# Optimization experiments

Hardware: AMD Instinct MI355X
Metric: run time of the kernel (lower is better)

Reference implementation:

```python
import jax, jax.numpy as jnp
import numpy as np

N_HEAD = 16
N_KV = 4
HEAD_DIM = 64
QK_SCALE = 1.2
VE_GATE_CH = 12


def rms_norm(x):
    # F.rms_norm with default eps = finfo(dtype).eps, no learned scale
    eps = jnp.asarray(jnp.finfo(x.dtype).eps, x.dtype)
    return x * jax.lax.rsqrt(jnp.mean(x * x, axis=-1, keepdims=True) + eps)


def apply_rotary(x, cos, sin):
    # x: (B,T,H,D); cos/sin: (1,T,1,D//2)
    d = x.shape[-1] // 2
    x1, x2 = x[..., :d], x[..., d:]
    return jnp.concatenate([x1 * cos + x2 * sin, -x1 * sin + x2 * cos], axis=-1)


def setup_inputs() -> dict:
    key = jax.random.key(0)
    ks = jax.random.split(key, 8)
    B, T, C = 2, 2048, 1024
    x = jax.random.normal(ks[0], (B, T, C), jnp.float32)
    ve = jax.random.normal(ks[1], (B, T, N_KV * HEAD_DIM), jnp.float32)
    # realistic rotary tables for positions 0..T
    half = HEAD_DIM // 2
    inv_freq = 1.0 / (10000.0 ** (np.arange(half, dtype=np.float64) / half))
    ang = np.arange(T)[:, None] * inv_freq[None, :]
    cos = jnp.asarray(np.cos(ang), jnp.float32)[None, :, None, :]
    sin = jnp.asarray(np.sin(ang), jnp.float32)[None, :, None, :]
    s = 0.02
    Wq = jax.random.normal(ks[2], (N_HEAD * HEAD_DIM, C), jnp.float32) * s
    Wk = jax.random.normal(ks[3], (N_KV * HEAD_DIM, C), jnp.float32) * s
    Wv = jax.random.normal(ks[4], (N_KV * HEAD_DIM, C), jnp.float32) * s
    Wo = jax.random.normal(ks[5], (C, C), jnp.float32) * s
    Wg = jax.random.normal(ks[6], (N_KV, VE_GATE_CH), jnp.float32) * s
    return dict(x=x, ve=ve, cos=cos, sin=sin, Wq=Wq, Wk=Wk, Wv=Wv, Wo=Wo,
                Wg=Wg, window_left=1024)


def reference(x, ve, cos, sin, Wq, Wk, Wv, Wo, Wg, window_left):
    B, T, C = x.shape
    G = N_HEAD // N_KV  # GQA group size
    q = (x @ Wq.T).reshape(B, T, N_HEAD, HEAD_DIM)
    k = (x @ Wk.T).reshape(B, T, N_KV, HEAD_DIM)
    v = (x @ Wv.T).reshape(B, T, N_KV, HEAD_DIM)
    # sigmoid-gated value-embedding mixing
    gate = 3.0 * jax.nn.sigmoid(x[..., :VE_GATE_CH] @ Wg.T)  # (B,T,N_KV)
    v = v + gate[..., None] * ve.reshape(B, T, N_KV, HEAD_DIM)
    # RoPE -> RMSNorm -> qk_scale on both q and k
    q = rms_norm(apply_rotary(q, cos, sin)) * QK_SCALE
    k = rms_norm(apply_rotary(k, cos, sin)) * QK_SCALE
    # GQA attention with causal + sliding window (flash default scale 1/sqrt(d))
    qg = q.reshape(B, T, N_KV, G, HEAD_DIM)
    scale = 1.0 / jnp.sqrt(jnp.asarray(HEAD_DIM, q.dtype))
    scores = jnp.einsum('bqkgd,bskd->bkgqs', qg, k) * scale  # (B,N_KV,G,T,T)
    i = jnp.arange(T)[:, None]
    j = jnp.arange(T)[None, :]
    mask = (j <= i) & (i - j <= window_left)
    scores = jnp.where(mask, scores, jnp.asarray(-1e30, scores.dtype))
    attn = jax.nn.softmax(scores, axis=-1)
    y = jnp.einsum('bkgqs,bskd->bqkgd', attn, v).reshape(B, T, N_HEAD * HEAD_DIM)
    return y @ Wo.T
```

## Files before the change

kernel.cpp:

```cpp
#include <hip/hip_runtime.h>
#include <hip/hip_bf16.h>

#define B_ 2
#define T_ 2048
#define C_ 1024
#define NH 16
#define NKV 4
#define HD 64
#define NQKV 1536
#define KVB 64

typedef __attribute__((ext_vector_type(4))) float f32x4;
typedef __attribute__((ext_vector_type(8))) short bf16x8;
typedef __attribute__((ext_vector_type(4))) short bf16x4;

__device__ __forceinline__ unsigned short f2bf(float f) {
  __hip_bfloat16 h = __float2bfloat16(f);
  unsigned short u;
  __builtin_memcpy(&u, &h, 2);
  return u;
}

__device__ __forceinline__ void gload16(const void* g, void* l) {
  __builtin_amdgcn_global_load_lds(
      (const __attribute__((address_space(1))) void*)g,
      (__attribute__((address_space(3))) void*)l, 16, 0, 0);
}

__device__ __forceinline__ unsigned cvtpk(float lo, float hi_) {
  unsigned w;
  asm("v_cvt_pk_bf16_f32 %0, %1, %2" : "=v"(w) : "v"(lo), "v"(hi_));
  return w;
}

#define NX4  1048576
#define NW4  262144
#define NK4  65536
#define O1 (NX4)
#define O2 (O1 + NW4)
#define O3 (O2 + NK4)
#define O4 (O3 + NK4)
#define OT (O4 + NW4)

__global__ __launch_bounds__(256) void conv_all(
    const float* __restrict__ x, const float* __restrict__ wq, const float* __restrict__ wk,
    const float* __restrict__ wv, const float* __restrict__ wo,
    unsigned short* __restrict__ xb, unsigned short* __restrict__ wqkvb,
    unsigned short* __restrict__ wob) {
  int i = blockIdx.x * blockDim.x + threadIdx.x;
  const int stride = gridDim.x * blockDim.x;
  for (; i < OT; i += stride) {
    const float* src;
    unsigned short* dst;
    int j;
    if (i < O1)      { src = x;  dst = xb;                    j = i; }
    else if (i < O2) { src = wq; dst = wqkvb;                 j = i - O1; }
    else if (i < O3) { src = wk; dst = wqkvb + 1024 * 1024;   j = i - O2; }
    else if (i < O4) { src = wv; dst = wqkvb + 1280 * 1024;   j = i - O3; }
    else             { src = wo; dst = wob;                   j = i - O4; }
    const float4 v = reinterpret_cast<const float4*>(src)[j];
    ushort4 o;
    o.x = f2bf(v.x); o.y = f2bf(v.y); o.z = f2bf(v.z); o.w = f2bf(v.w);
    reinterpret_cast<ushort4*>(dst)[j] = o;
  }
}

#define BK 64

__global__ __launch_bounds__(256) void gemm_qkv(
    const unsigned short* __restrict__ A, const unsigned short* __restrict__ Bw,
    const float* __restrict__ x, const float* __restrict__ ve,
    const float* __restrict__ cosb, const float* __restrict__ sinb,
    const float* __restrict__ Wg,
    unsigned short* __restrict__ Qn, unsigned short* __restrict__ Kn,
    unsigned short* __restrict__ Vt) {
  constexpr int BMT = 128, MI = 4, NI = 2, K = 1024;
  __shared__ char smem[50176];
  unsigned short* AlB = (unsigned short*)smem;
  unsigned short* BlB = (unsigned short*)(smem + 32768);
  const int tid = threadIdx.x;
  const int lane = tid & 63;
  const int wid = tid >> 6;
  const int r = lane & 15, g = lane >> 4;
  const int wm = (wid >> 1) * 64, wn = (wid & 1) * 32;
  const int bm0 = blockIdx.y * BMT, bn0 = blockIdx.x * 64;
  const int lrow = lane >> 3;
  const int lcol = ((lane & 7) ^ lrow) * 8;
  const unsigned short* Asrc = A + (size_t)(bm0 + wid * 32 + lrow) * K + lcol;
  const unsigned short* Bsrc = Bw + (size_t)(bn0 + wid * 16 + lrow) * K + lcol;
  const int fsw = (r & 7) << 4;
  f32x4 acc[MI][NI] = {};

  auto stage = [&](int k0, int buf) {
#pragma unroll
    for (int i = 0; i < 4; ++i)
      gload16(Asrc + (size_t)(i * 8) * K + k0, AlB + buf * 8192 + (wid * 32 + i * 8) * BK);
#pragma unroll
    for (int i = 0; i < 2; ++i)
      gload16(Bsrc + (size_t)(i * 8) * K + k0, BlB + buf * 4096 + (wid * 16 + i * 8) * BK);
  };

  stage(0, 0);
  __syncthreads();
  const int nt = K / BK;
  for (int t = 0; t < nt; ++t) {
    const int cur = t & 1;
    if (t + 1 < nt) stage((t + 1) * BK, cur ^ 1);
    const char* Ac = (const char*)(AlB + cur * 8192);
    const char* Bc = (const char*)(BlB + cur * 4096);
    bf16x8 af[MI][2], bfr[NI][2];
#pragma unroll
    for (int mi = 0; mi < MI; ++mi)
#pragma unroll
      for (int s = 0; s < 2; ++s)
        af[mi][s] = *reinterpret_cast<const bf16x8*>(
            Ac + (wm + mi * 16 + r) * 128 + ((s * 64 + g * 16) ^ fsw));
#pragma unroll
    for (int ni = 0; ni < NI; ++ni)
#pragma unroll
      for (int s = 0; s < 2; ++s)
        bfr[ni][s] = *reinterpret_cast<const bf16x8*>(
            Bc + (wn + ni * 16 + r) * 128 + ((s * 64 + g * 16) ^ fsw));
#pragma unroll
    for (int s = 0; s < 2; ++s)
#pragma unroll
      for (int mi = 0; mi < MI; ++mi)
#pragma unroll
        for (int ni = 0; ni < NI; ++ni)
          acc[mi][ni] = __builtin_amdgcn_mfma_f32_16x16x32_bf16(af[mi][s], bfr[ni][s],
                                                                acc[mi][ni], 0, 0, 0);
    __syncthreads();
  }
  float* Cl = (float*)smem;
  unsigned short* Vst = (unsigned short*)(smem + 33280);
#pragma unroll
  for (int mi = 0; mi < MI; ++mi)
#pragma unroll
    for (int ni = 0; ni < NI; ++ni)
#pragma unroll
      for (int e = 0; e < 4; ++e)
        Cl[(wm + mi * 16 + g * 4 + e) * 65 + wn + ni * 16 + r] = acc[mi][ni][e];
  __syncthreads();
  const int head = blockIdx.x;
  const int trow = tid >> 1, half = tid & 1;
  const int tg = bm0 + trow;
  const int b = tg >> 11, t = tg & 2047;
  if (head < 20) {
    float r1[16], r2[16];
    float sq = 0.f;
#pragma unroll
    for (int i = 0; i < 16; ++i) {
      const int d = half * 16 + i;
      const float x1 = Cl[trow * 65 + d];
      const float x2 = Cl[trow * 65 + d + 32];
      const float c = cosb[t * 32 + d];
      const float s = sinb[t * 32 + d];
      r1[i] = x1 * c + x2 * s;
      r2[i] = x2 * c - x1 * s;
      sq += r1[i] * r1[i] + r2[i] * r2[i];
    }
    sq += __shfl_xor(sq, 1);
    const float sc = rsqrtf(sq * (1.0f / 64.0f) + 1.1920929e-7f) *
                     ((head < 16) ? 0.21640425613334453f : 1.2f);
    unsigned short* dst = (head < 16)
        ? Qn + (((size_t)b * NH + head) * T_ + t) * HD
        : Kn + (((size_t)b * NKV + (head - 16)) * T_ + t) * HD;
#pragma unroll
    for (int i4 = 0; i4 < 4; ++i4) {
      ushort4 w1, w2;
      w1.x = f2bf(r1[i4 * 4 + 0] * sc); w1.y = f2bf(r1[i4 * 4 + 1] * sc);
      w1.z = f2bf(r1[i4 * 4 + 2] * sc); w1.w = f2bf(r1[i4 * 4 + 3] * sc);
      w2.x = f2bf(r2[i4 * 4 + 0] * sc); w2.y = f2bf(r2[i4 * 4 + 1] * sc);
      w2.z = f2bf(r2[i4 * 4 + 2] * sc); w2.w = f2bf(r2[i4 * 4 + 3] * sc);
      *reinterpret_cast<ushort4*>(dst + half * 16 + i4 * 4) = w1;
      *reinterpret_cast<ushort4*>(dst + half * 16 + 32 + i4 * 4) = w2;
    }
  } else {
    const int kv = head - 20;
    float dot = 0.f;
#pragma unroll
    for (int i = 0; i < 12; ++i) dot += x[(size_t)tg * C_ + i] * Wg[kv * 12 + i];
    const float gate = 3.0f / (1.0f + __expf(-dot));
    const float* vsrc = ve + (size_t)tg * (NKV * HD) + kv * HD;
#pragma unroll
    for (int i = 0; i < 32; ++i) {
      const int d = half * 32 + i;
      Vst[d * 128 + trow] = f2bf(Cl[trow * 65 + d] + gate * vsrc[d]);
    }
    __syncthreads();
    const int dd = tid >> 2, t0 = (tid & 3) * 32;
    unsigned short* vd = Vt + (((size_t)b * NKV + kv) * HD + dd) * T_ + (bm0 & 2047) + t0;
    const unsigned short* vs2 = Vst + dd * 128 + t0;
#pragma unroll
    for (int i = 0; i < 4; ++i)
      *reinterpret_cast<bf16x8*>(vd + i * 8) = *reinterpret_cast<const bf16x8*>(vs2 + i * 8);
  }
}

template <int BMT, int BNT, bool OUTBF>
__global__ __launch_bounds__(256) void gemm_bt(const unsigned short* __restrict__ A,
                                               const unsigned short* __restrict__ Bw,
                                               void* __restrict__ Cv, int M, int N, int K) {
  constexpr int MI = BMT / 32;
  constexpr int NI = BNT / 32;
  __shared__ unsigned short Al[2][BMT * BK];
  __shared__ unsigned short Bl[2][BNT * BK];
  const int tid = threadIdx.x;
  const int lane = tid & 63;
  const int wid = tid >> 6;
  const int r = lane & 15, g = lane >> 4;
  const int wm = (wid >> 1) * (BMT / 2), wn = (wid & 1) * (BNT / 2);
  const int bm0 = blockIdx.y * BMT, bn0 = blockIdx.x * BNT;
  const int lrow = lane >> 3;
  const int lcol = ((lane & 7) ^ lrow) * 8;
  const unsigned short* Asrc = A + (size_t)(bm0 + wid * (BMT / 4) + lrow) * K + lcol;
  const unsigned short* Bsrc = Bw + (size_t)(bn0 + wid * (BNT / 4) + lrow) * K + lcol;
  const int fsw = (r & 7) << 4;
  f32x4 acc[MI][NI] = {};

  auto stage = [&](int k0, int buf) {
#pragma unroll
    for (int i = 0; i < BMT / 32; ++i)
      gload16(Asrc + (size_t)(i * 8) * K + k0, Al[buf] + (wid * (BMT / 4) + i * 8) * BK);
#pragma unroll
    for (int i = 0; i < BNT / 32; ++i)
      gload16(Bsrc + (size_t)(i * 8) * K + k0, Bl[buf] + (wid * (BNT / 4) + i * 8) * BK);
  };

  stage(0, 0);
  __syncthreads();
  const int nt = K / BK;
  for (int t = 0; t < nt; ++t) {
    const int cur = t & 1;
    if (t + 1 < nt) stage((t + 1) * BK, cur ^ 1);
    const char* Ac = (const char*)Al[cur];
    const char* Bc = (const char*)Bl[cur];
    bf16x8 af[MI][2], bfr[NI][2];
#pragma unroll
    for (int mi = 0; mi < MI; ++mi)
#pragma unroll
      for (int s = 0; s < 2; ++s)
        af[mi][s] = *reinterpret_cast<const bf16x8*>(
            Ac + (wm + mi * 16 + r) * 128 + ((s * 64 + g * 16) ^ fsw));
#pragma unroll
    for (int ni = 0; ni < NI; ++ni)
#pragma unroll
      for (int s = 0; s < 2; ++s)
        bfr[ni][s] = *reinterpret_cast<const bf16x8*>(
            Bc + (wn + ni * 16 + r) * 128 + ((s * 64 + g * 16) ^ fsw));
#pragma unroll
    for (int s = 0; s < 2; ++s)
#pragma unroll
      for (int mi = 0; mi < MI; ++mi)
#pragma unroll
        for (int ni = 0; ni < NI; ++ni)
          acc[mi][ni] = __builtin_amdgcn_mfma_f32_16x16x32_bf16(af[mi][s], bfr[ni][s],
                                                                acc[mi][ni], 0, 0, 0);
    __syncthreads();
  }
#pragma unroll
  for (int mi = 0; mi < MI; ++mi)
#pragma unroll
    for (int ni = 0; ni < NI; ++ni) {
      const int row = bm0 + wm + mi * 16 + g * 4;
      const int col = bn0 + wn + ni * 16 + r;
#pragma unroll
      for (int e = 0; e < 4; ++e) {
        if (OUTBF)
          ((unsigned short*)Cv)[(size_t)(row + e) * N + col] = f2bf(acc[mi][ni][e]);
        else
          ((float*)Cv)[(size_t)(row + e) * N + col] = acc[mi][ni][e];
      }
    }
}

__global__ __launch_bounds__(256, 4) void attn_fwd(
    const unsigned short* __restrict__ Qn, const unsigned short* __restrict__ Kn,
    const unsigned short* __restrict__ Vt, unsigned short* __restrict__ Y,
    const int* __restrict__ wlp) {
  __shared__ unsigned short Kl[2][KVB * 64];
  __shared__ unsigned short Vl[2][64 * KVB];
  __shared__ unsigned short Pl[4][16 * 64];
  const int j = blockIdx.x, h = blockIdx.y, b = blockIdx.z;
  const int kvh = h >> 2;
  const int tid = threadIdx.x;
  const int wid = tid >> 6, lane = tid & 63;
  const int r = lane & 15, g = lane >> 4;
  const int wl = *wlp;
  const unsigned short* Kb = Kn + (size_t)(b * NKV + kvh) * T_ * HD;
  const unsigned short* Vb = Vt + (size_t)(b * NKV + kvh) * HD * T_;
  const int srow = tid >> 3;
  const int scolb = (tid & 7) * 16;
  const int sdst = srow * 128 + (scolb ^ ((srow & 7) << 4));
  const unsigned short* Ksrc0 = Kb + (size_t)srow * HD + (scolb >> 1);
  const unsigned short* Ksrc1 = Kb + (size_t)(srow + 32) * HD + (scolb >> 1);
  const unsigned short* Vsrc0 = Vb + (size_t)srow * T_ + (scolb >> 1);
  const unsigned short* Vsrc1 = Vb + (size_t)(srow + 32) * T_ + (scolb >> 1);
  char* Pwb = (char*)Pl[wid];
  const int swz = (r & 7) << 4;
  const int ksw = swz;
  const int nseg = (j < 8) ? 2 : 1;

  for (int seg = 0; seg < nseg; ++seg) {
    const int qt = (j < 8) ? (seg ? 15 - j : j) : j + 8;
    const int q0 = qt * 64;
    const int qs = q0 + wid * 16;
    const int q = qs + r;
    const unsigned short* Qb = Qn + ((size_t)(b * NH + h) * T_ + qs) * HD;
    const bf16x8 qf0 = *reinterpret_cast<const bf16x8*>(Qb + r * HD + g * 8);
    const bf16x8 qf1 = *reinterpret_cast<const bf16x8*>(Qb + r * HD + 32 + g * 8);
    float lrun = 0.f;
    f32x4 o[4] = {};
    int slo = q0 - wl; if (slo < 0) slo = 0;
    slo &= ~63;
    const int send = q0 + 63;

    bf16x8 ska, skb, sva, svb;
    ska = *reinterpret_cast<const bf16x8*>(Ksrc0 + (size_t)slo * HD);
    skb = *reinterpret_cast<const bf16x8*>(Ksrc1 + (size_t)slo * HD);
    sva = *reinterpret_cast<const bf16x8*>(Vsrc0 + slo);
    svb = *reinterpret_cast<const bf16x8*>(Vsrc1 + slo);
    {
      char* Kd = (char*)Kl[0]; char* Vd = (char*)Vl[0];
      *reinterpret_cast<bf16x8*>(Kd + sdst) = ska;
      *reinterpret_cast<bf16x8*>(Kd + 32 * 128 + sdst) = skb;
      *reinterpret_cast<bf16x8*>(Vd + sdst) = sva;
      *reinterpret_cast<bf16x8*>(Vd + 32 * 128 + sdst) = svb;
    }
    __syncthreads();

    int cur = 0;
    for (int sb = slo; sb <= send; sb += KVB) {
      const bool has_next = (sb + KVB <= send);
      if (has_next) {
        const int nb = sb + KVB;
        ska = *reinterpret_cast<const bf16x8*>(Ksrc0 + (size_t)nb * HD);
        skb = *reinterpret_cast<const bf16x8*>(Ksrc1 + (size_t)nb * HD);
        sva = *reinterpret_cast<const bf16x8*>(Vsrc0 + nb);
        svb = *reinterpret_cast<const bf16x8*>(Vsrc1 + nb);
      }
      {
        const char* Kc = (const char*)Kl[cur];
        const char* Vc = (const char*)Vl[cur];
        float sv[16];
        __builtin_amdgcn_s_setprio(1);
#pragma unroll
        for (int sub = 0; sub < 4; ++sub) {
          const int rowb = (sub * 16 + r) * 128;
          bf16x8 kf0 = *reinterpret_cast<const bf16x8*>(Kc + rowb + ((g * 16) ^ ksw));
          bf16x8 kf1 = *reinterpret_cast<const bf16x8*>(Kc + rowb + ((64 + g * 16) ^ ksw));
          f32x4 z = {};
          z = __builtin_amdgcn_mfma_f32_16x16x32_bf16(kf0, qf0, z, 0, 0, 0);
          z = __builtin_amdgcn_mfma_f32_16x16x32_bf16(kf1, qf1, z, 0, 0, 0);
#pragma unroll
          for (int e = 0; e < 4; ++e) sv[sub * 4 + e] = z[e];
        }
        __builtin_amdgcn_s_setprio(0);
        if (sb + 63 > qs || sb < qs + 15 - wl) {
#pragma unroll
          for (int i = 0; i < 16; ++i) {
            const int s_ = sb + (i >> 2) * 16 + g * 4 + (i & 3);
            const bool ok = (unsigned)(q - s_) <= (unsigned)wl;
            sv[i] = ok ? sv[i] : -__builtin_inff();
          }
        }
        float pe[16];
        float ps = 0.f;
#pragma unroll
        for (int i = 0; i < 16; ++i) {
          pe[i] = __builtin_amdgcn_exp2f(sv[i] - 17.0f);
          ps += pe[i];
        }
        lrun += ps;
#pragma unroll
        for (int sub = 0; sub < 4; ++sub) {
          unsigned w2[2];
          w2[0] = cvtpk(pe[sub * 4 + 0], pe[sub * 4 + 1]);
          w2[1] = cvtpk(pe[sub * 4 + 2], pe[sub * 4 + 3]);
          bf16x4 w;
          __builtin_memcpy(&w, w2, 8);
          *reinterpret_cast<bf16x4*>(Pwb + ((r * 128 + sub * 32 + g * 8) ^ swz)) = w;
        }
        asm volatile("s_waitcnt lgkmcnt(0)" ::: "memory");
        __builtin_amdgcn_s_setprio(1);
#pragma unroll
        for (int c = 0; c < 2; ++c) {
          const bf16x8 pf = *reinterpret_cast<const bf16x8*>(Pwb + ((r * 128 + c * 64 + g * 16) ^ swz));
#pragma unroll
          for (int dt = 0; dt < 4; ++dt) {
            const int vrow = (dt * 16 + r) * 128;
            const bf16x8 vf = *reinterpret_cast<const bf16x8*>(Vc + vrow + ((c * 64 + g * 16) ^ ksw));
            o[dt] = __builtin_amdgcn_mfma_f32_16x16x32_bf16(vf, pf, o[dt], 0, 0, 0);
          }
        }
        __builtin_amdgcn_s_setprio(0);
      }
      if (has_next) {
        char* Kd = (char*)Kl[cur ^ 1]; char* Vd = (char*)Vl[cur ^ 1];
        *reinterpret_cast<bf16x8*>(Kd + sdst) = ska;
        *reinterpret_cast<bf16x8*>(Kd + 32 * 128 + sdst) = skb;
        *reinterpret_cast<bf16x8*>(Vd + sdst) = sva;
        *reinterpret_cast<bf16x8*>(Vd + 32 * 128 + sdst) = svb;
      }
      __syncthreads();
      cur ^= 1;
    }
    lrun += __shfl_xor(lrun, 16);
    lrun += __shfl_xor(lrun, 32);
    const float inv = 1.0f / lrun;
    unsigned short* Yb = Y + ((size_t)(b * T_) + qs + r) * (NH * HD) + h * HD;
#pragma unroll
    for (int dt = 0; dt < 4; ++dt)
#pragma unroll
      for (int e = 0; e < 4; ++e)
        Yb[dt * 16 + g * 4 + e] = f2bf(o[dt][e] * inv);
  }
}

extern "C" void kernel_launch(void* const* d_in, const int* in_sizes, int n_in,
                              void* d_out, int out_size, void* d_ws, size_t ws_size,
                              hipStream_t stream) {
  const float* x    = (const float*)d_in[0];
  const float* ve   = (const float*)d_in[1];
  const float* cosb = (const float*)d_in[2];
  const float* sinb = (const float*)d_in[3];
  const float* Wq   = (const float*)d_in[4];
  const float* Wk   = (const float*)d_in[5];
  const float* Wv   = (const float*)d_in[6];
  const float* Wo   = (const float*)d_in[7];
  const float* Wg   = (const float*)d_in[8];
  const int*   wlp  = (const int*)d_in[9];

  char* ws = (char*)d_ws;
  unsigned short* xb    = (unsigned short*)ws; ws += (size_t)4096 * 1024 * 2;
  unsigned short* wqkvb = (unsigned short*)ws; ws += (size_t)1536 * 1024 * 2;
  unsigned short* wob   = (unsigned short*)ws; ws += (size_t)1024 * 1024 * 2;
  unsigned short* Qn    = (unsigned short*)ws; ws += (size_t)B_ * NH * T_ * HD * 2;
  unsigned short* Kn    = (unsigned short*)ws; ws += (size_t)B_ * NKV * T_ * HD * 2;
  unsigned short* Vt    = (unsigned short*)ws; ws += (size_t)B_ * NKV * HD * T_ * 2;
  unsigned short* yb    = (unsigned short*)ws; ws += (size_t)4096 * 1024 * 2;

  conv_all<<<dim3(2048), dim3(256), 0, stream>>>(x, Wq, Wk, Wv, Wo, xb, wqkvb, wob);

  gemm_qkv<<<dim3(NQKV / 64, 4096 / 128), dim3(256), 0, stream>>>(
      xb, wqkvb, x, ve, cosb, sinb, Wg, Qn, Kn, Vt);

  attn_fwd<<<dim3(24, NH, B_), dim3(256), 0, stream>>>(Qn, Kn, Vt, yb, wlp);

  gemm_bt<128, 64, false><<<dim3(1024 / 64, 4096 / 128), dim3(256), 0, stream>>>(
      yb, wob, d_out, 4096, 1024, 1024);
}
```

Measured before the change: 76.26 us.

## Fuse x fp32-to-bf16 conversion into QKV GEMM A-tile loading

New measurement: 84.34 us. 1.11x slower.

```diff
diff --git a/kernel.cpp b/kernel.cpp
--- a/kernel.cpp
+++ b/kernel.cpp
@@ -33,31 +33,27 @@
   return w;
 }
 
-#define NX4  1048576
 #define NW4  262144
 #define NK4  65536
-#define O1 (NX4)
-#define O2 (O1 + NW4)
-#define O3 (O2 + NK4)
-#define O4 (O3 + NK4)
-#define OT (O4 + NW4)
+#define W1 (NW4)
+#define W2 (W1 + NK4)
+#define W3 (W2 + NK4)
+#define WT (W3 + NW4)
 
 __global__ __launch_bounds__(256) void conv_all(
-    const float* __restrict__ x, const float* __restrict__ wq, const float* __restrict__ wk,
+    const float* __restrict__ wq, const float* __restrict__ wk,
     const float* __restrict__ wv, const float* __restrict__ wo,
-    unsigned short* __restrict__ xb, unsigned short* __restrict__ wqkvb,
-    unsigned short* __restrict__ wob) {
+    unsigned short* __restrict__ wqkvb, unsigned short* __restrict__ wob) {
   int i = blockIdx.x * blockDim.x + threadIdx.x;
   const int stride = gridDim.x * blockDim.x;
-  for (; i < OT; i += stride) {
+  for (; i < WT; i += stride) {
     const float* src;
     unsigned short* dst;
     int j;
-    if (i < O1)      { src = x;  dst = xb;                    j = i; }
-    else if (i < O2) { src = wq; dst = wqkvb;                 j = i - O1; }
-    else if (i < O3) { src = wk; dst = wqkvb + 1024 * 1024;   j = i - O2; }
-    else if (i < O4) { src = wv; dst = wqkvb + 1280 * 1024;   j = i - O3; }
-    else             { src = wo; dst = wob;                   j = i - O4; }
+    if (i < W1)      { src = wq; dst = wqkvb;                 j = i; }
+    else if (i < W2) { src = wk; dst = wqkvb + 1024 * 1024;   j = i - W1; }
+    else if (i < W3) { src = wv; dst = wqkvb + 1280 * 1024;   j = i - W2; }
+    else             { src = wo; dst = wob;                   j = i - W3; }
     const float4 v = reinterpret_cast<const float4*>(src)[j];
     ushort4 o;
     o.x = f2bf(v.x); o.y = f2bf(v.y); o.z = f2bf(v.z); o.w = f2bf(v.w);
@@ -68,8 +64,8 @@
 #define BK 64
 
 __global__ __launch_bounds__(256) void gemm_qkv(
-    const unsigned short* __restrict__ A, const unsigned short* __restrict__ Bw,
-    const float* __restrict__ x, const float* __restrict__ ve,
+    const float* __restrict__ x, const unsigned short* __restrict__ Bw,
+    const float* __restrict__ ve,
     const float* __restrict__ cosb, const float* __restrict__ sinb,
     const float* __restrict__ Wg,
     unsigned short* __restrict__ Qn, unsigned short* __restrict__ Kn,
@@ -85,27 +81,49 @@
   const int wm = (wid >> 1) * 64, wn = (wid & 1) * 32;
   const int bm0 = blockIdx.y * BMT, bn0 = blockIdx.x * 64;
   const int lrow = lane >> 3;
-  const int lcol = ((lane & 7) ^ lrow) * 8;
-  const unsigned short* Asrc = A + (size_t)(bm0 + wid * 32 + lrow) * K + lcol;
+  const int lslot = lane & 7;
+  const int lcol = (lslot ^ lrow) * 8;
   const unsigned short* Bsrc = Bw + (size_t)(bn0 + wid * 16 + lrow) * K + lcol;
   const int fsw = (r & 7) << 4;
   f32x4 acc[MI][NI] = {};
 
-  auto stage = [&](int k0, int buf) {
-#pragma unroll
-    for (int i = 0; i < 4; ++i)
-      gload16(Asrc + (size_t)(i * 8) * K + k0, AlB + buf * 8192 + (wid * 32 + i * 8) * BK);
+  float4 a0[4], a1[4];
+  const float* Axs = x + (size_t)(bm0 + wid * 32 + lrow) * K + lslot * 8;
+  const int adst0 = (wid * 32 + lrow) * 128 + ((lslot * 16) ^ (lrow << 4));
+
+  auto loadA = [&](int k0) {
+#pragma unroll
+    for (int i = 0; i < 4; ++i) {
+      const float* src = Axs + (size_t)(i * 8) * K + k0;
+      a0[i] = *reinterpret_cast<const float4*>(src);
+      a1[i] = *reinterpret_cast<const float4*>(src + 4);
+    }
+  };
+  auto writeA = [&](int buf) {
+    char* base = (char*)(AlB + buf * 8192);
+#pragma unroll
+    for (int i = 0; i < 4; ++i) {
+      unsigned w[4];
+      w[0] = cvtpk(a0[i].x, a0[i].y); w[1] = cvtpk(a0[i].z, a0[i].w);
+      w[2] = cvtpk(a1[i].x, a1[i].y); w[3] = cvtpk(a1[i].z, a1[i].w);
+      bf16x8 v; __builtin_memcpy(&v, w, 16);
+      *reinterpret_cast<bf16x8*>(base + adst0 + i * 8 * 128) = v;
+    }
+  };
+  auto stageB = [&](int k0, int buf) {
 #pragma unroll
     for (int i = 0; i < 2; ++i)
       gload16(Bsrc + (size_t)(i * 8) * K + k0, BlB + buf * 4096 + (wid * 16 + i * 8) * BK);
   };
 
-  stage(0, 0);
+  loadA(0);
+  stageB(0, 0);
+  writeA(0);
   __syncthreads();
   const int nt = K / BK;
   for (int t = 0; t < nt; ++t) {
     const int cur = t & 1;
-    if (t + 1 < nt) stage((t + 1) * BK, cur ^ 1);
+    if (t + 1 < nt) { loadA((t + 1) * BK); stageB((t + 1) * BK, cur ^ 1); }
     const char* Ac = (const char*)(AlB + cur * 8192);
     const char* Bc = (const char*)(BlB + cur * 4096);
     bf16x8 af[MI][2], bfr[NI][2];
@@ -129,6 +147,7 @@
         for (int ni = 0; ni < NI; ++ni)
           acc[mi][ni] = __builtin_amdgcn_mfma_f32_16x16x32_bf16(af[mi][s], bfr[ni][s],
                                                                 acc[mi][ni], 0, 0, 0);
+    if (t + 1 < nt) writeA(cur ^ 1);
     __syncthreads();
   }
   float* Cl = (float*)smem;
@@ -432,7 +451,6 @@
   const int*   wlp  = (const int*)d_in[9];
 
   char* ws = (char*)d_ws;
-  unsigned short* xb    = (unsigned short*)ws; ws += (size_t)4096 * 1024 * 2;
   unsigned short* wqkvb = (unsigned short*)ws; ws += (size_t)1536 * 1024 * 2;
   unsigned short* wob   = (unsigned short*)ws; ws += (size_t)1024 * 1024 * 2;
   unsigned short* Qn    = (unsigned short*)ws; ws += (size_t)B_ * NH * T_ * HD * 2;
@@ -440,10 +458,10 @@
   unsigned short* Vt    = (unsigned short*)ws; ws += (size_t)B_ * NKV * HD * T_ * 2;
   unsigned short* yb    = (unsigned short*)ws; ws += (size_t)4096 * 1024 * 2;
 
-  conv_all<<<dim3(2048), dim3(256), 0, stream>>>(x, Wq, Wk, Wv, Wo, xb, wqkvb, wob);
+  conv_all<<<dim3(1024), dim3(256), 0, stream>>>(Wq, Wk, Wv, Wo, wqkvb, wob);
 
   gemm_qkv<<<dim3(NQKV / 64, 4096 / 128), dim3(256), 0, stream>>>(
-      xb, wqkvb, x, ve, cosb, sinb, Wg, Qn, Kn, Vt);
+      x, wqkvb, ve, cosb, sinb, Wg, Qn, Kn, Vt);
 
   attn_fwd<<<dim3(24, NH, B_), dim3(256), 0, stream>>>(Qn, Kn, Vt, yb, wlp);
 
```
